# Optimization experiments

Hardware: AMD Instinct MI355X
Metric: run time of the kernel (lower is better)

## Reference

```python
import jax, jax.numpy as jnp
import numpy as np

NOISE_DIM = 32
HIDDEN_DIM = 256
DATA_DIM = 2
TEMP = 0.05
N = 16384
DIAG_PENALTY = 1e6


def _cdist(a, b):
    # Euclidean pairwise distance [Na, Nb], safe sqrt (zero grad at d==0 like torch.cdist)
    d2 = (jnp.sum(a * a, -1)[:, None] + jnp.sum(b * b, -1)[None, :]
          - 2.0 * (a @ b.T))
    d2 = jnp.maximum(d2, 0.0)
    safe = jnp.where(d2 > 0, d2, 1.0)
    return jnp.where(d2 > 0, jnp.sqrt(safe), 0.0)


def setup_inputs() -> dict:
    key = jax.random.key(0)
    ks = jax.random.split(key, 12)
    pos = jax.random.normal(ks[0], (N, DATA_DIM), dtype=jnp.float32)
    z = jax.random.normal(ks[1], (N, NOISE_DIM), dtype=jnp.float32)
    def lin(k, fan_in, fan_out):
        bound = 1.0 / np.sqrt(fan_in)
        k1, k2 = jax.random.split(k)
        W = jax.random.uniform(k1, (fan_in, fan_out), minval=-bound, maxval=bound, dtype=jnp.float32)
        b = jax.random.uniform(k2, (fan_out,), minval=-bound, maxval=bound, dtype=jnp.float32)
        return W, b
    W1, b1 = lin(ks[2], NOISE_DIM, HIDDEN_DIM)
    W2, b2 = lin(ks[3], HIDDEN_DIM, HIDDEN_DIM)
    W3, b3 = lin(ks[4], HIDDEN_DIM, HIDDEN_DIM)
    W4, b4 = lin(ks[5], HIDDEN_DIM, HIDDEN_DIM)
    W5, b5 = lin(ks[6], HIDDEN_DIM, DATA_DIM)
    return {"pos": pos, "z": z, "W1": W1, "b1": b1, "W2": W2, "b2": b2,
            "W3": W3, "b3": b3, "W4": W4, "b4": b4, "W5": W5, "b5": b5}


def reference(pos, z, W1, b1, W2, b2, W3, b3, W4, b4, W5, b5):
    # SELU MLP generator
    h = jax.nn.selu(z @ W1 + b1)
    h = jax.nn.selu(h @ W2 + b2)
    h = jax.nn.selu(h @ W3 + b3)
    h = jax.nn.selu(h @ W4 + b4)
    gen = h @ W5 + b5  # [N, D]

    y_pos = jax.lax.stop_gradient(pos)
    y_neg = jax.lax.stop_gradient(gen)

    dist_pos = _cdist(gen, y_pos)  # [N, N]
    dist_neg = _cdist(gen, y_neg)  # [N, N]
    dist_neg = dist_neg + jnp.eye(gen.shape[0], dtype=gen.dtype) * DIAG_PENALTY

    energy_pos = -TEMP * jax.nn.logsumexp(-dist_pos / TEMP, axis=1)
    energy_neg = TEMP * jax.nn.logsumexp(-dist_neg / TEMP, axis=1)
    return energy_pos + energy_neg  # [N]
```

## Files before the change

kernel.cpp:

```cpp
#include <hip/hip_runtime.h>
#include <hip/hip_bf16.h>

#define N_PTS 16384
#define TEMP_F 0.05f

typedef __attribute__((ext_vector_type(8))) short bf16x8;
typedef __attribute__((ext_vector_type(4))) float f32x4;

__device__ __forceinline__ float selu_f(float x) {
    const float scale = 1.0507009873554805f;
    const float alpha = 1.6732632423543772f;
    return x > 0.f ? scale * x : scale * alpha * (__expf(x) - 1.f);
}

__device__ __forceinline__ float fast_sqrtf(float x) {
#if __has_builtin(__builtin_amdgcn_sqrtf)
    return __builtin_amdgcn_sqrtf(x);
#else
    return sqrtf(x);
#endif
}

__device__ __forceinline__ float fast_exp2f(float x) {
#if __has_builtin(__builtin_amdgcn_exp2f)
    return __builtin_amdgcn_exp2f(x);
#else
    return exp2f(x);
#endif
}

__device__ __forceinline__ float fast_log2f(float x) {
#if __has_builtin(__builtin_amdgcn_logf)
    return __builtin_amdgcn_logf(x);
#else
    return log2f(x);
#endif
}

__device__ __forceinline__ f32x4 mfma_bf16(bf16x8 a, bf16x8 b, f32x4 c) {
    return __builtin_amdgcn_mfma_f32_16x16x32_bf16(a, b, c, 0, 0, 0);
}

__device__ __forceinline__ void split_bf16(float v, unsigned short& hi, unsigned short& lo) {
    unsigned u = __float_as_uint(v);
    hi = (unsigned short)(u >> 16);
    float ah = __uint_as_float(u & 0xFFFF0000u);
    lo = (unsigned short)(__float_as_uint(v - ah) >> 16);
}

__global__ __launch_bounds__(256) void pack_kernel(
    const float* __restrict__ W1, const float* __restrict__ W2,
    const float* __restrict__ W3, const float* __restrict__ W4,
    unsigned short* __restrict__ pk)
{
    int idx = blockIdx.x * 256 + threadIdx.x;
    if (idx >= 25600) return;
    const float* src;
    unsigned short *dh, *dl;
    int nt, kc, l, KC;
    if (idx < 1024) {
        src = W1; dh = pk; dl = pk + 8192; KC = 1;
        nt = idx >> 6; kc = 0; l = idx & 63;
    } else {
        int t2 = idx - 1024;
        int ly = t2 >> 13;
        int r2 = t2 & 8191;
        src = (ly == 0) ? W2 : (ly == 1) ? W3 : W4;
        dh = pk + 16384 + ly * 131072;
        dl = dh + 65536;
        KC = 8;
        nt = r2 >> 9; kc = (r2 >> 6) & 7; l = r2 & 63;
    }
    int lr = l & 15, lq = l >> 4;
    int n = nt * 16 + lr;
    bf16x8 hv, lv;
    #pragma unroll
    for (int e = 0; e < 8; e++) {
        int k = kc * 32 + lq * 8 + e;
        float v = src[k * 256 + n];
        unsigned short hb, lb;
        split_bf16(v, hb, lb);
        hv[e] = (short)hb; lv[e] = (short)lb;
    }
    int base = ((nt * KC + kc) * 64 + l) * 8;
    *(bf16x8*)(dh + base) = hv;
    *(bf16x8*)(dl + base) = lv;
}

__global__ __launch_bounds__(512) void mlp_mfma_kernel(
    const float* __restrict__ z,
    const unsigned short* __restrict__ pk,
    const float* __restrict__ b1, const float* __restrict__ b2,
    const float* __restrict__ b3, const float* __restrict__ b4,
    const float* __restrict__ W5, const float* __restrict__ b5,
    float* __restrict__ gen)
{
    __shared__ __align__(16) unsigned short Hh[32 * 256];
    __shared__ __align__(16) unsigned short Hl[32 * 256];

    const int t  = threadIdx.x;
    const int l  = t & 63;
    const int wv = t >> 6;
    const int lr = l & 15;
    const int lq = l >> 4;
    const int row0 = blockIdx.x * 32;
    const int bro  = blockIdx.x & 7;
    const int wp   = (wv + (blockIdx.x >> 3)) & 7;

    f32x4 acc[2][2];

    {
        bf16x8 ah[2], al[2];
        #pragma unroll
        for (int m = 0; m < 2; m++) {
            const float* zp = z + (row0 + m * 16 + lr) * 32 + lq * 8;
            f32x4 z0 = *(const f32x4*)(zp);
            f32x4 z1 = *(const f32x4*)(zp + 4);
            #pragma unroll
            for (int e = 0; e < 8; e++) {
                float v = (e < 4) ? z0[e] : z1[e - 4];
                unsigned short hb, lb;
                split_bf16(v, hb, lb);
                ah[m][e] = (short)hb; al[m][e] = (short)lb;
            }
        }
        #pragma unroll
        for (int n2 = 0; n2 < 2; n2++) {
            float bv = b1[wp * 32 + n2 * 16 + lr];
            #pragma unroll
            for (int m = 0; m < 2; m++) acc[m][n2] = (f32x4){bv, bv, bv, bv};
        }
        const bf16x8* B1h = (const bf16x8*)(pk);
        const bf16x8* B1l = (const bf16x8*)(pk + 8192);
        #pragma unroll
        for (int n2 = 0; n2 < 2; n2++) {
            int nt = wp * 2 + n2;
            bf16x8 bh = B1h[nt * 64 + l];
            bf16x8 bl = B1l[nt * 64 + l];
            #pragma unroll
            for (int m = 0; m < 2; m++) {
                acc[m][n2] = mfma_bf16(ah[m], bh, acc[m][n2]);
                acc[m][n2] = mfma_bf16(ah[m], bl, acc[m][n2]);
                acc[m][n2] = mfma_bf16(al[m], bh, acc[m][n2]);
            }
        }
        #pragma unroll
        for (int m = 0; m < 2; m++) {
            #pragma unroll
            for (int n2 = 0; n2 < 2; n2++) {
                #pragma unroll
                for (int r = 0; r < 4; r++) {
                    float v = selu_f(acc[m][n2][r]);
                    int rowo = m * 16 + lq * 4 + r;
                    int n = wp * 32 + n2 * 16 + lr;
                    int o = (2 * n) ^ ((rowo & 7) << 4);
                    unsigned short hb, lb;
                    split_bf16(v, hb, lb);
                    Hh[rowo * 256 + (o >> 1)] = hb;
                    Hl[rowo * 256 + (o >> 1)] = lb;
                }
            }
        }
    }
    __syncthreads();

    #pragma unroll 1
    for (int ly = 0; ly < 3; ly++) {
        const unsigned short* wbase = pk + 16384 + ly * 131072;
        const bf16x8* Bh = (const bf16x8*)(wbase);
        const bf16x8* Bl = (const bf16x8*)(wbase + 65536);
        const float* bb = (ly == 0) ? b2 : (ly == 1) ? b3 : b4;
        #pragma unroll
        for (int n2 = 0; n2 < 2; n2++) {
            float bv = bb[wp * 32 + n2 * 16 + lr];
            #pragma unroll
            for (int m = 0; m < 2; m++) acc[m][n2] = (f32x4){bv, bv, bv, bv};
        }
        #pragma unroll 4
        for (int kci = 0; kci < 8; kci++) {
            int kc = (kci + bro) & 7;
            bf16x8 ah[2], al[2];
            #pragma unroll
            for (int m = 0; m < 2; m++) {
                int arow = m * 16 + lr;
                int o = (kc * 64 + lq * 16) ^ ((arow & 7) << 4);
                ah[m] = *(const bf16x8*)(Hh + arow * 256 + (o >> 1));
                al[m] = *(const bf16x8*)(Hl + arow * 256 + (o >> 1));
            }
            #pragma unroll
            for (int n2 = 0; n2 < 2; n2++) {
                int nt = wp * 2 + n2;
                bf16x8 bh = Bh[(nt * 8 + kc) * 64 + l];
                bf16x8 bl = Bl[(nt * 8 + kc) * 64 + l];
                #pragma unroll
                for (int m = 0; m < 2; m++) {
                    acc[m][n2] = mfma_bf16(ah[m], bh, acc[m][n2]);
                    acc[m][n2] = mfma_bf16(ah[m], bl, acc[m][n2]);
                    acc[m][n2] = mfma_bf16(al[m], bh, acc[m][n2]);
                }
            }
        }
        __syncthreads();
        #pragma unroll
        for (int m = 0; m < 2; m++) {
            #pragma unroll
            for (int n2 = 0; n2 < 2; n2++) {
                #pragma unroll
                for (int r = 0; r < 4; r++) {
                    float v = selu_f(acc[m][n2][r]);
                    int rowo = m * 16 + lq * 4 + r;
                    int n = wp * 32 + n2 * 16 + lr;
                    int o = (2 * n) ^ ((rowo & 7) << 4);
                    unsigned short hb, lb;
                    split_bf16(v, hb, lb);
                    Hh[rowo * 256 + (o >> 1)] = hb;
                    Hl[rowo * 256 + (o >> 1)] = lb;
                }
            }
        }
        __syncthreads();
    }

    if (t < 64) {
        int row = t & 31;
        int d = t >> 5;
        float sum = b5[d];
        #pragma unroll 4
        for (int k = 0; k < 256; k += 8) {
            int o = (2 * k) ^ ((row & 7) << 4);
            bf16x8 hh = *(const bf16x8*)(Hh + row * 256 + (o >> 1));
            bf16x8 ll = *(const bf16x8*)(Hl + row * 256 + (o >> 1));
            #pragma unroll
            for (int e = 0; e < 8; e++) {
                float hv = __uint_as_float(((unsigned)(unsigned short)hh[e]) << 16)
                         + __uint_as_float(((unsigned)(unsigned short)ll[e]) << 16);
                sum = fmaf(hv, W5[(k + e) * 2 + d], sum);
            }
        }
        gen[(row0 + row) * 2 + d] = sum;
    }
}

__global__ __launch_bounds__(1024) void mlp_kernel(
    const float* __restrict__ z,
    const float* __restrict__ W1, const float* __restrict__ b1,
    const float* __restrict__ W2, const float* __restrict__ b2,
    const float* __restrict__ W3, const float* __restrict__ b3,
    const float* __restrict__ W4, const float* __restrict__ b4,
    const float* __restrict__ W5, const float* __restrict__ b5,
    float* __restrict__ gen)
{
    __shared__ float h[256 * 64];

    const int t = threadIdx.x;
    const int r = t & 63;
    const int w = __builtin_amdgcn_readfirstlane(t >> 6);
    const int c0 = w * 16;
    const int row0 = blockIdx.x * 64;

    #pragma unroll
    for (int e = 0; e < 2; e++) {
        int f  = t + e * 1024;
        int rz = f >> 5;
        int kz = f & 31;
        h[kz * 64 + rz] = z[(row0 + rz) * 32 + kz];
    }
    __syncthreads();

    float acc[16];

    #pragma unroll
    for (int j = 0; j < 16; j++) acc[j] = b1[c0 + j];
    #pragma unroll 8
    for (int k = 0; k < 32; k++) {
        float hv = h[k * 64 + r];
        const float* Wr = W1 + k * 256 + c0;
        #pragma unroll
        for (int j = 0; j < 16; j++) acc[j] = fmaf(hv, Wr[j], acc[j]);
    }
    __syncthreads();
    #pragma unroll
    for (int j = 0; j < 16; j++) h[(c0 + j) * 64 + r] = selu_f(acc[j]);
    __syncthreads();

    for (int layer = 0; layer < 3; layer++) {
        const float* W = (layer == 0) ? W2 : (layer == 1) ? W3 : W4;
        const float* b = (layer == 0) ? b2 : (layer == 1) ? b3 : b4;
        #pragma unroll
        for (int j = 0; j < 16; j++) acc[j] = b[c0 + j];
        #pragma unroll 4
        for (int k = 0; k < 256; k++) {
            float hv = h[k * 64 + r];
            const float* Wr = W + k * 256 + c0;
            #pragma unroll
            for (int j = 0; j < 16; j++) acc[j] = fmaf(hv, Wr[j], acc[j]);
        }
        __syncthreads();
        #pragma unroll
        for (int j = 0; j < 16; j++) h[(c0 + j) * 64 + r] = selu_f(acc[j]);
        __syncthreads();
    }

    float p0 = 0.f, p1 = 0.f;
    #pragma unroll
    for (int kk = 0; kk < 16; kk++) {
        int k = c0 + kk;
        float hv = h[k * 64 + r];
        p0 = fmaf(hv, W5[k * 2 + 0], p0);
        p1 = fmaf(hv, W5[k * 2 + 1], p1);
    }
    __syncthreads();
    h[(0 * 16 + w) * 64 + r] = p0;
    h[(1 * 16 + w) * 64 + r] = p1;
    __syncthreads();
    if (t < 128) {
        int d  = t >> 6;
        int rr = t & 63;
        float sum = b5[d];
        #pragma unroll
        for (int ss = 0; ss < 16; ss++) sum += h[(d * 16 + ss) * 64 + rr];
        gen[(row0 + rr) * 2 + d] = sum;
    }
}

__global__ __launch_bounds__(512) void energy_kernel(
    const float* __restrict__ gen,
    const float* __restrict__ pos,
    float* __restrict__ out)
{
    __shared__ float4 sp[512];
    __shared__ float4 sg[512];

    const int t  = threadIdx.x;
    const int s  = t & 31;
    const int rl = t >> 5;
    const int i  = blockIdx.x * 16 + rl;
    const int diagBase = ((blockIdx.x * 16) >> 10) << 10;

    const float2 q = ((const float2*)gen)[i];

    const float cL2 = 28.853900817779268f;
    const float Tl2 = 0.034657359027997264f;
    const float cB  = 57.707801635558536f;

    float p0 = 0.f, p1 = 0.f, n0 = 0.f, n1 = 0.f;

    for (int base = 0; base < N_PTS; base += 1024) {
        __syncthreads();
        sp[t] = ((const float4*)pos)[base / 2 + t];
        sg[t] = ((const float4*)gen)[base / 2 + t];
        __syncthreads();
        if (base == diagBase) {
            #pragma unroll 4
            for (int u = 0; u < 16; u++) {
                int j = base + 2 * (s + 32 * u);
                float4 pp = sp[s + 32 * u];
                float4 gg = sg[s + 32 * u];
                float dx = q.x - pp.x, dy = q.y - pp.y;
                float d  = fast_sqrtf(fmaf(dx, dx, dy * dy));
                p0 += fast_exp2f(fmaf(-cL2, d, cB));
                dx = q.x - pp.z; dy = q.y - pp.w;
                d  = fast_sqrtf(fmaf(dx, dx, dy * dy));
                p1 += fast_exp2f(fmaf(-cL2, d, cB));
                dx = q.x - gg.x; dy = q.y - gg.y;
                d  = fast_sqrtf(fmaf(dx, dx, dy * dy));
                float e0 = fast_exp2f(fmaf(-cL2, d, cB));
                n0 += (j == i) ? 0.f : e0;
                dx = q.x - gg.z; dy = q.y - gg.w;
                d  = fast_sqrtf(fmaf(dx, dx, dy * dy));
                float e1 = fast_exp2f(fmaf(-cL2, d, cB));
                n1 += (j + 1 == i) ? 0.f : e1;
            }
        } else {
            #pragma unroll 4
            for (int u = 0; u < 16; u++) {
                float4 pp = sp[s + 32 * u];
                float4 gg = sg[s + 32 * u];
                float dx = q.x - pp.x, dy = q.y - pp.y;
                float d  = fast_sqrtf(fmaf(dx, dx, dy * dy));
                p0 += fast_exp2f(fmaf(-cL2, d, cB));
                dx = q.x - pp.z; dy = q.y - pp.w;
                d  = fast_sqrtf(fmaf(dx, dx, dy * dy));
                p1 += fast_exp2f(fmaf(-cL2, d, cB));
                dx = q.x - gg.x; dy = q.y - gg.y;
                d  = fast_sqrtf(fmaf(dx, dx, dy * dy));
                n0 += fast_exp2f(fmaf(-cL2, d, cB));
                dx = q.x - gg.z; dy = q.y - gg.w;
                d  = fast_sqrtf(fmaf(dx, dx, dy * dy));
                n1 += fast_exp2f(fmaf(-cL2, d, cB));
            }
        }
    }

    float sump = p0 + p1;
    float sumn = n0 + n1;
    #pragma unroll
    for (int m = 1; m < 32; m <<= 1) {
        sump += __shfl_xor(sump, m, 32);
        sumn += __shfl_xor(sumn, m, 32);
    }

    if (s == 0) {
        out[i] = Tl2 * (fast_log2f(sumn) - fast_log2f(sump));
    }
}

extern "C" void kernel_launch(void* const* d_in, const int* in_sizes, int n_in,
                              void* d_out, int out_size, void* d_ws, size_t ws_size,
                              hipStream_t stream) {
    const float* pos = (const float*)d_in[0];
    const float* z   = (const float*)d_in[1];
    const float* W1  = (const float*)d_in[2];
    const float* b1  = (const float*)d_in[3];
    const float* W2  = (const float*)d_in[4];
    const float* b2  = (const float*)d_in[5];
    const float* W3  = (const float*)d_in[6];
    const float* b3  = (const float*)d_in[7];
    const float* W4  = (const float*)d_in[8];
    const float* b4  = (const float*)d_in[9];
    const float* W5  = (const float*)d_in[10];
    const float* b5  = (const float*)d_in[11];

    float* gen = (float*)d_ws;
    unsigned short* pk = (unsigned short*)((char*)d_ws + 131072);
    float* outp = (float*)d_out;
    const size_t WS_NEEDED = 131072 + (size_t)409600 * 2;

    if (ws_size >= WS_NEEDED) {
        pack_kernel<<<100, 256, 0, stream>>>(W1, W2, W3, W4, pk);
        mlp_mfma_kernel<<<N_PTS / 32, 512, 0, stream>>>(z, pk, b1, b2, b3, b4,
                                                        W5, b5, gen);
    } else {
        mlp_kernel<<<N_PTS / 64, 1024, 0, stream>>>(z, W1, b1, W2, b2, W3, b3,
                                                    W4, b4, W5, b5, gen);
    }
    energy_kernel<<<N_PTS / 16, 512, 0, stream>>>(gen, pos, outp);
}
```

Baseline: 237.7 us.

## Bin points spatially and prune distant tiles in energy logsumexp

Sorts pos and gen points into a 32x32 grid via histogram, scan and scatter, then computes per-64-point tile bounding boxes. Each 16-query block keeps only the tiles whose minimum distance is within the best tile's maximum distance plus a cutoff, and sums exp terms only over those. This aims to remove most of the dense N^2 distance/exp work, whose far terms underflow at the low temperature. It adds several small launches and atomics, and truncates negligible terms as an approximation.

```diff
diff --git a/kernel.cpp b/kernel.cpp
--- a/kernel.cpp
+++ b/kernel.cpp
@@ -3,6 +3,7 @@
 
 #define N_PTS 16384
 #define TEMP_F 0.05f
+#define RCUT 0.8f
 
 typedef __attribute__((ext_vector_type(8))) short bf16x8;
 typedef __attribute__((ext_vector_type(4))) float f32x4;
@@ -46,6 +47,14 @@
     hi = (unsigned short)(u >> 16);
     float ah = __uint_as_float(u & 0xFFFF0000u);
     lo = (unsigned short)(__float_as_uint(v - ah) >> 16);
+}
+
+__device__ __forceinline__ int cellOf(float x, float y) {
+    int cx = (int)floorf((x + 6.4f) * 2.5f);
+    int cy = (int)floorf((y + 6.4f) * 2.5f);
+    cx = min(31, max(0, cx));
+    cy = min(31, max(0, cy));
+    return cy * 32 + cx;
 }
 
 __global__ __launch_bounds__(256) void pack_kernel(
@@ -320,6 +329,190 @@
         #pragma unroll
         for (int ss = 0; ss < 16; ss++) sum += h[(d * 16 + ss) * 64 + rr];
         gen[(row0 + rr) * 2 + d] = sum;
+    }
+}
+
+__global__ __launch_bounds__(512) void zero_kernel(int* __restrict__ cnt) {
+    int t = blockIdx.x * 512 + threadIdx.x;
+    if (t < 2048) cnt[t] = 0;
+}
+
+__global__ __launch_bounds__(512) void hist_kernel(
+    const float* __restrict__ pos, const float* __restrict__ gen,
+    int* __restrict__ cnt)
+{
+    int idx = blockIdx.x * 512 + threadIdx.x;
+    int side = idx >> 14, i = idx & 16383;
+    const float* src = side ? gen : pos;
+    int cell = cellOf(src[2 * i], src[2 * i + 1]);
+    atomicAdd(cnt + side * 1024 + cell, 1);
+}
+
+__global__ __launch_bounds__(1024) void scan_kernel(
+    const int* __restrict__ cnt, int* __restrict__ cursor)
+{
+    __shared__ int buf[1024];
+    int t = threadIdx.x;
+    const int* c = cnt + blockIdx.x * 1024;
+    int own = c[t];
+    buf[t] = own;
+    __syncthreads();
+    for (int off = 1; off < 1024; off <<= 1) {
+        int u = (t >= off) ? buf[t - off] : 0;
+        __syncthreads();
+        buf[t] += u;
+        __syncthreads();
+    }
+    cursor[blockIdx.x * 1024 + t] = buf[t] - own;
+}
+
+__global__ __launch_bounds__(512) void scatter_kernel(
+    const float* __restrict__ pos, const float* __restrict__ gen,
+    int* __restrict__ cursor,
+    float2* __restrict__ posS, float2* __restrict__ genS,
+    int* __restrict__ genOrig)
+{
+    int idx = blockIdx.x * 512 + threadIdx.x;
+    int side = idx >> 14, i = idx & 16383;
+    const float* src = side ? gen : pos;
+    float x = src[2 * i], y = src[2 * i + 1];
+    int cell = cellOf(x, y);
+    int p = atomicAdd(cursor + side * 1024 + cell, 1);
+    if (side) { genS[p] = make_float2(x, y); genOrig[p] = i; }
+    else      { posS[p] = make_float2(x, y); }
+}
+
+__global__ __launch_bounds__(256) void bbox_kernel(
+    const float2* __restrict__ posS, const float2* __restrict__ genS,
+    float4* __restrict__ posB, float4* __restrict__ genB)
+{
+    const float2* src = blockIdx.x ? genS : posS;
+    float4* dst = blockIdx.x ? genB : posB;
+    int st = threadIdx.x;
+    float x0 = 1e30f, y0 = 1e30f, x1 = -1e30f, y1 = -1e30f;
+    for (int e = 0; e < 64; e++) {
+        float2 p = src[st * 64 + e];
+        x0 = fminf(x0, p.x); x1 = fmaxf(x1, p.x);
+        y0 = fminf(y0, p.y); y1 = fmaxf(y1, p.y);
+    }
+    dst[st] = make_float4(x0, y0, x1, y1);
+}
+
+__global__ __launch_bounds__(512) void energy_binned(
+    const float2* __restrict__ posS, const float2* __restrict__ genS,
+    const int* __restrict__ genOrig,
+    const float4* __restrict__ posB, const float4* __restrict__ genB,
+    float* __restrict__ out)
+{
+    __shared__ float qb[4];
+    __shared__ float wmin[8];
+    __shared__ float dub2s[2];
+    __shared__ int   wcnt[8], wbase[8], nPG[2];
+    __shared__ unsigned short listP[256], listG[256];
+
+    const int t  = threadIdx.x;
+    const int b  = blockIdx.x;
+    const int s  = t & 31;
+    const int rl = t >> 5;
+    const int i_s = b * 16 + rl;
+
+    const float2 q = genS[i_s];
+
+    if (t == 0) {
+        float x0 = 1e30f, y0 = 1e30f, x1 = -1e30f, y1 = -1e30f;
+        for (int r = 0; r < 16; r++) {
+            float2 p = genS[b * 16 + r];
+            x0 = fminf(x0, p.x); x1 = fmaxf(x1, p.x);
+            y0 = fminf(y0, p.y); y1 = fmaxf(y1, p.y);
+        }
+        qb[0] = x0; qb[1] = y0; qb[2] = x1; qb[3] = y1;
+    }
+    __syncthreads();
+    const float qx0 = qb[0], qy0 = qb[1], qx1 = qb[2], qy1 = qb[3];
+
+    const int stl  = t & 255;
+    const int side = t >> 8;
+    float4 bb = side ? genB[stl] : posB[stl];
+    float dxo = fmaxf(fmaxf(bb.x - qx1, qx0 - bb.z), 0.f);
+    float dyo = fmaxf(fmaxf(bb.y - qy1, qy0 - bb.w), 0.f);
+    float md2 = dxo * dxo + dyo * dyo;
+    float mxx = fmaxf(bb.z - qx0, qx1 - bb.x);
+    float mxy = fmaxf(bb.w - qy0, qy1 - bb.y);
+    float Md2 = mxx * mxx + mxy * mxy;
+    {
+        float w = Md2;
+        #pragma unroll
+        for (int m = 1; m < 64; m <<= 1) w = fminf(w, __shfl_xor(w, m));
+        if ((t & 63) == 0) wmin[t >> 6] = w;
+    }
+    __syncthreads();
+    if (t == 0) {
+        dub2s[0] = fminf(fminf(wmin[0], wmin[1]), fminf(wmin[2], wmin[3]));
+        dub2s[1] = fminf(fminf(wmin[4], wmin[5]), fminf(wmin[6], wmin[7]));
+    }
+    __syncthreads();
+    float thr = fast_sqrtf(dub2s[side]) + RCUT;
+    bool keep = md2 <= thr * thr;
+    unsigned long long mk = __ballot(keep);
+    int wv = t >> 6;
+    if ((t & 63) == 0) wcnt[wv] = __popcll(mk);
+    __syncthreads();
+    if (t == 0) {
+        int a = 0;
+        for (int w = 0; w < 4; w++) { wbase[w] = a; a += wcnt[w]; }
+        nPG[0] = a; a = 0;
+        for (int w = 4; w < 8; w++) { wbase[w] = a; a += wcnt[w]; }
+        nPG[1] = a;
+    }
+    __syncthreads();
+    if (keep) {
+        int p = wbase[wv] + __popcll(mk & ((1ull << (t & 63)) - 1ull));
+        if (side == 0) listP[p] = (unsigned short)stl;
+        else           listG[p] = (unsigned short)stl;
+    }
+    __syncthreads();
+    const int nP = nPG[0], nG = nPG[1];
+
+    const float cL2 = 28.853900817779268f;
+    const float Tl2 = 0.034657359027997264f;
+    const float cB  = 57.707801635558536f;
+
+    const float4* posS4 = (const float4*)posS;
+    const float4* genS4 = (const float4*)genS;
+
+    float sump = 0.f, sumn = 0.f;
+
+    for (int idx = 0; idx < nP; idx++) {
+        int st = listP[idx];
+        float4 pp = posS4[st * 32 + s];
+        float dx = q.x - pp.x, dy = q.y - pp.y;
+        float d  = fast_sqrtf(fmaf(dx, dx, dy * dy));
+        sump += fast_exp2f(fmaf(-cL2, d, cB));
+        dx = q.x - pp.z; dy = q.y - pp.w;
+        d  = fast_sqrtf(fmaf(dx, dx, dy * dy));
+        sump += fast_exp2f(fmaf(-cL2, d, cB));
+    }
+    for (int idx = 0; idx < nG; idx++) {
+        int st = listG[idx];
+        float4 gg = genS4[st * 32 + s];
+        int j0 = st * 64 + 2 * s;
+        float dx = q.x - gg.x, dy = q.y - gg.y;
+        float d  = fast_sqrtf(fmaf(dx, dx, dy * dy));
+        float e0 = fast_exp2f(fmaf(-cL2, d, cB));
+        sumn += (j0 == i_s) ? 0.f : e0;
+        dx = q.x - gg.z; dy = q.y - gg.w;
+        d  = fast_sqrtf(fmaf(dx, dx, dy * dy));
+        float e1 = fast_exp2f(fmaf(-cL2, d, cB));
+        sumn += (j0 + 1 == i_s) ? 0.f : e1;
+    }
+
+    #pragma unroll
+    for (int m = 1; m < 32; m <<= 1) {
+        sump += __shfl_xor(sump, m, 32);
+        sumn += __shfl_xor(sumn, m, 32);
+    }
+    if (s == 0) {
+        out[genOrig[i_s]] = Tl2 * (fast_log2f(sumn) - fast_log2f(sump));
     }
 }
 
@@ -421,12 +614,22 @@
     const float* W5  = (const float*)d_in[10];
     const float* b5  = (const float*)d_in[11];
 
-    float* gen = (float*)d_ws;
-    unsigned short* pk = (unsigned short*)((char*)d_ws + 131072);
+    char* ws = (char*)d_ws;
+    float*          gen     = (float*)(ws);
+    unsigned short* pk      = (unsigned short*)(ws + 131072);
+    float2*         posS    = (float2*)(ws + 950272);
+    float2*         genS    = (float2*)(ws + 1081344);
+    int*            genOrig = (int*)   (ws + 1212416);
+    float4*         posB    = (float4*)(ws + 1277952);
+    float4*         genB    = (float4*)(ws + 1282048);
+    int*            cnt     = (int*)   (ws + 1286144);
+    int*            cursor  = (int*)   (ws + 1294336);
     float* outp = (float*)d_out;
-    const size_t WS_NEEDED = 131072 + (size_t)409600 * 2;
-
-    if (ws_size >= WS_NEEDED) {
+
+    const size_t WS_MFMA   = 950272;
+    const size_t WS_BINNED = 1302528;
+
+    if (ws_size >= WS_MFMA) {
         pack_kernel<<<100, 256, 0, stream>>>(W1, W2, W3, W4, pk);
         mlp_mfma_kernel<<<N_PTS / 32, 512, 0, stream>>>(z, pk, b1, b2, b3, b4,
                                                         W5, b5, gen);
@@ -434,5 +637,17 @@
         mlp_kernel<<<N_PTS / 64, 1024, 0, stream>>>(z, W1, b1, W2, b2, W3, b3,
                                                     W4, b4, W5, b5, gen);
     }
-    energy_kernel<<<N_PTS / 16, 512, 0, stream>>>(gen, pos, outp);
-}
+
+    if (ws_size >= WS_BINNED) {
+        zero_kernel<<<4, 512, 0, stream>>>(cnt);
+        hist_kernel<<<64, 512, 0, stream>>>(pos, gen, cnt);
+        scan_kernel<<<2, 1024, 0, stream>>>(cnt, cursor);
+        scatter_kernel<<<64, 512, 0, stream>>>(pos, gen, cursor,
+                                               posS, genS, genOrig);
+        bbox_kernel<<<2, 256, 0, stream>>>(posS, genS, posB, genB);
+        energy_binned<<<N_PTS / 16, 512, 0, stream>>>(posS, genS, genOrig,
+                                                      posB, genB, outp);
+    } else {
+        energy_kernel<<<N_PTS / 16, 512, 0, stream>>>(gen, pos, outp);
+    }
+}
```

Result: slower. 509.8 us (+114.5%).
